# Optimization experiments

Measured on AMD Instinct MI355X. Metric: run time of the kernel, lower is better.

## Reference

```python
import jax, jax.numpy as jnp
import numpy as np


def setup_inputs() -> dict:
    key = jax.random.key(0)
    k1, k2, k3 = jax.random.split(key, 3)
    B, H, W, D, C, F = 2, 96, 128, 64, 32, 32
    images = jax.random.normal(k1, (B, H, W, D, C), dtype=jnp.float32)
    base_plane = jax.random.randint(k2, (B, H, W, 1), 0, 16, dtype=jnp.int32)
    kernel = jax.random.normal(k3, (3, 3, 3, C, F), dtype=jnp.float32) * 0.05
    default_value = jnp.zeros((), dtype=jnp.float32)
    return {"images": images, "base_plane": base_plane,
            "kernel": kernel, "default_value": default_value}


def _sparse_conv3d(images, base_plane, kernel, default_value):
    # images: [B,H,W,D,C] stored depth band per pixel, starting at base_plane
    # base_plane: [B,H,W,1] int, kernel: [KH,KW,KD,C,F]
    B, H, W, D, C = images.shape
    KH, KW, KD, _, F = kernel.shape
    ph, pw, pd = KH // 2, KW // 2, KD // 2
    bp = base_plane[..., 0]  # [B,H,W]

    # pad spatially once; out-of-image neighbors read default_value
    img_pad = jnp.pad(images, ((0, 0), (ph, ph), (pw, pw), (0, 0), (0, 0)))
    bp_pad = jnp.pad(bp, ((0, 0), (ph, ph), (pw, pw)))
    sp_valid_pad = jnp.pad(jnp.ones((H, W), dtype=bool),
                           ((ph, ph), (pw, pw)))

    d_grid = jnp.arange(D)[None, None, None, :]  # [1,1,1,D]
    out = jnp.zeros((B, H, W, D, F), dtype=images.dtype)

    for kh in range(KH):
        for kw in range(KW):
            img_s = img_pad[:, kh:kh + H, kw:kw + W]          # [B,H,W,D,C]
            bp_s = bp_pad[:, kh:kh + H, kw:kw + W]            # [B,H,W]
            sp_valid = sp_valid_pad[kh:kh + H, kw:kw + W]     # [H,W]
            for kd in range(KD):
                # neighbor stored-depth index = (d + bp) + (kd-pd) - bp_neighbor
                idx = d_grid + (bp - bp_s)[:, :, :, None] + (kd - pd)  # [B,H,W,D]
                valid = (idx >= 0) & (idx < D) & sp_valid[None, :, :, None]
                g = jnp.take_along_axis(
                    img_s, jnp.clip(idx, 0, D - 1)[..., None], axis=3)
                val = jnp.where(valid[..., None], g, default_value)
                out = out + jnp.einsum('bhwdc,cf->bhwdf', val,
                                       kernel[kh, kw, kd])
    return out


def reference(images, base_plane, kernel, default_value):
    return _sparse_conv3d(images, base_plane, kernel, default_value)
```

## Files before the change

kernel.cpp:

```cpp
#include <hip/hip_runtime.h>
#include <hip/hip_bf16.h>

#define Bn 2
#define Hn 96
#define Wn 128
#define Dn 64
#define Cn 32
#define Fn 32
#define TH 2
#define TW 8
#define CW (TW + 2)
#define NCOLS (4 * CW)
#define COLSZ (Dn * Cn)

typedef short bf16x8 __attribute__((ext_vector_type(8)));
typedef float f32x4  __attribute__((ext_vector_type(4)));

__device__ __forceinline__ ushort f2bf(float x) {
    __hip_bfloat16 h = __float2bfloat16(x);
    return *reinterpret_cast<ushort*>(&h);
}

__device__ __forceinline__ int swz_off(int r, int slot) {
    return r * 32 + ((slot ^ ((r >> 1) & 3)) << 3);
}

__global__ void prep_kT(const float* __restrict__ kern, ushort* __restrict__ kT) {
    const int e = blockIdx.x * 256 + threadIdx.x;
    if (e >= 30 * Cn * Fn) return;
    const int c  = e & 31;
    const int f  = (e >> 5) & 31;
    const int kk = e >> 10;
    kT[e] = (kk < 27) ? f2bf(kern[kk * (Cn * Fn) + c * Fn + f]) : (ushort)0;
}

__global__ __launch_bounds__(1024, 4) void sconv3d_mfma(
    const float*  __restrict__ img,
    const int*    __restrict__ bp,
    const float*  __restrict__ kern,
    const ushort* __restrict__ kT,
    const float*  __restrict__ dvp,
    float*        __restrict__ out)
{
    __shared__ ushort colS[NCOLS * COLSZ];

    const int blk = blockIdx.x;
    const int wt  = blk % (Wn / TW);
    const int ht  = (blk / (Wn / TW)) % (Hn / TH);
    const int b   = blk / ((Wn / TW) * (Hn / TH));
    const int h0  = ht * TH;
    const int w0  = wt * TW;

    const int tid  = threadIdx.x;
    const int lane = tid & 63;
    const int wave = tid >> 6;
    const int ph   = wave >> 3;
    const int pw   = wave & 7;
    const int h    = h0 + ph;
    const int w    = w0 + pw;

    const int lrow = lane & 15;
    const int lgrp = lane >> 4;

    const float dv  = *dvp;
    const int   bpc = bp[(b * Hn + h) * Wn + w];

    int  sh[9];
    bool tv[9];
#pragma unroll
    for (int kh = 0; kh < 3; ++kh)
#pragma unroll
        for (int kw = 0; kw < 3; ++kw) {
            const int hh = h - 1 + kh;
            const int ww = w - 1 + kw;
            const bool v = (hh >= 0) && (hh < Hn) && (ww >= 0) && (ww < Wn);
            tv[kh * 3 + kw] = v;
            sh[kh * 3 + kw] = v ? (bpc - bp[(b * Hn + hh) * Wn + ww]) : 0;
        }

#pragma unroll
    for (int it = 0; it < 20; ++it) {
        const int e  = it * 1024 + tid;
        const int j  = e >> 9;
        const int sl = e & 511;
        const int hh = h0 - 1 + j / CW;
        const int ww = w0 - 1 + j % CW;
        const bool v = (hh >= 0) && (hh < Hn) && (ww >= 0) && (ww < Wn);
        float4 x = make_float4(0.f, 0.f, 0.f, 0.f);
        if (v) x = *(const float4*)(img +
                     (size_t)((b * Hn + hh) * Wn + ww) * COLSZ + sl * 4);
        ushort4 u;
        u.x = f2bf(x.x); u.y = f2bf(x.y); u.z = f2bf(x.z); u.w = f2bf(x.w);
        *(ushort4*)&colS[j * COLSZ
                         + swz_off(sl >> 3, (sl >> 1) & 3) + (sl & 1) * 4] = u;
    }
    __syncthreads();

    f32x4 acc[4][2];
#pragma unroll
    for (int i = 0; i < 4; ++i)
#pragma unroll
        for (int j = 0; j < 2; ++j) acc[i][j] = (f32x4)0.f;

#pragma unroll
    for (int kh = 0; kh < 3; ++kh) {
#pragma unroll
        for (int kw = 0; kw < 3; ++kw) {
            const int t    = kh * 3 + kw;
            const int s    = sh[t];
            const int kkb  = tv[t] ? t * 3 : 27;
            const ushort* colp = &colS[((ph + kh) * CW + (pw + kw)) * COLSZ];
            bf16x8 bfr[3][2];
#pragma unroll
            for (int kd = 0; kd < 3; ++kd) {
                bfr[kd][0] = *(const bf16x8*)&kT[((kkb + kd) * Fn + lrow)      * Cn + lgrp * 8];
                bfr[kd][1] = *(const bf16x8*)&kT[((kkb + kd) * Fn + lrow + 16) * Cn + lgrp * 8];
            }
            __builtin_amdgcn_s_setprio(1);
#pragma unroll
            for (int kd = 0; kd < 3; ++kd) {
                const int i1 = 16 + lrow + s + kd - 1;
                const int o1 = swz_off(i1, lgrp);
                const bf16x8 a1 = *(const bf16x8*)&colp[o1];
                acc[1][0] = __builtin_amdgcn_mfma_f32_16x16x32_bf16(a1, bfr[kd][0], acc[1][0], 0, 0, 0);
                acc[1][1] = __builtin_amdgcn_mfma_f32_16x16x32_bf16(a1, bfr[kd][1], acc[1][1], 0, 0, 0);
                const bf16x8 a2 = *(const bf16x8*)&colp[o1 + 512];
                acc[2][0] = __builtin_amdgcn_mfma_f32_16x16x32_bf16(a2, bfr[kd][0], acc[2][0], 0, 0, 0);
                acc[2][1] = __builtin_amdgcn_mfma_f32_16x16x32_bf16(a2, bfr[kd][1], acc[2][1], 0, 0, 0);
                {
                    const bool vv = (i1 >= 16);
                    bf16x8 a0 = *(const bf16x8*)&colp[vv ? o1 - 512 : o1];
                    if (!vv) a0 = (bf16x8)0;
                    acc[0][0] = __builtin_amdgcn_mfma_f32_16x16x32_bf16(a0, bfr[kd][0], acc[0][0], 0, 0, 0);
                    acc[0][1] = __builtin_amdgcn_mfma_f32_16x16x32_bf16(a0, bfr[kd][1], acc[0][1], 0, 0, 0);
                }
                {
                    const bool vv = (i1 <= 31);
                    bf16x8 a3 = *(const bf16x8*)&colp[vv ? o1 + 1024 : o1];
                    if (!vv) a3 = (bf16x8)0;
                    acc[3][0] = __builtin_amdgcn_mfma_f32_16x16x32_bf16(a3, bfr[kd][0], acc[3][0], 0, 0, 0);
                    acc[3][1] = __builtin_amdgcn_mfma_f32_16x16x32_bf16(a3, bfr[kd][1], acc[3][1], 0, 0, 0);
                }
            }
            __builtin_amdgcn_s_setprio(0);
        }
    }

    if (dv != 0.0f) {
#pragma unroll
        for (int kh = 0; kh < 3; ++kh)
#pragma unroll
            for (int kw = 0; kw < 3; ++kw) {
                const bool sp = tv[kh * 3 + kw];
                const int  s  = sh[kh * 3 + kw];
                for (int kd = 0; kd < 3; ++kd) {
                    float ks0 = 0.f, ks1 = 0.f;
                    for (int c = 0; c < Cn; ++c) {
                        const float* kp = kern + (size_t)(((kh * 3 + kw) * 3 + kd) * Cn + c) * Fn;
                        ks0 += kp[lrow];
                        ks1 += kp[16 + lrow];
                    }
                    for (int dt = 0; dt < 4; ++dt)
                        for (int j = 0; j < 4; ++j) {
                            const int d   = dt * 16 + lgrp * 4 + j;
                            const int idx = d + s + kd - 1;
                            const bool valid = sp && (idx >= 0) && (idx < Dn);
                            if (!valid) { acc[dt][0][j] += dv * ks0; acc[dt][1][j] += dv * ks1; }
                        }
                }
            }
    }

    const size_t pixbase = ((size_t)(b * Hn + h) * Wn + w) * (Dn * Fn);
#pragma unroll
    for (int dt = 0; dt < 4; ++dt)
#pragma unroll
        for (int ft = 0; ft < 2; ++ft)
#pragma unroll
            for (int j = 0; j < 4; ++j) {
                const int d = dt * 16 + lgrp * 4 + j;
                const int f = ft * 16 + lrow;
                out[pixbase + d * Fn + f] = acc[dt][ft][j];
            }
}

extern "C" void kernel_launch(void* const* d_in, const int* in_sizes, int n_in,
                              void* d_out, int out_size, void* d_ws, size_t ws_size,
                              hipStream_t stream) {
    const float* img  = (const float*)d_in[0];
    const int*   bp   = (const int*)d_in[1];
    const float* kern = (const float*)d_in[2];
    const float* dvp  = (const float*)d_in[3];
    float* out = (float*)d_out;
    ushort* kT = (ushort*)d_ws;

    hipLaunchKernelGGL(prep_kT, dim3(120), dim3(256), 0, stream, kern, kT);

    const int nblk = Bn * (Hn / TH) * (Wn / TW);
    hipLaunchKernelGGL(sconv3d_mfma, dim3(nblk), dim3(1024), 0, stream,
                       img, bp, kern, kT, dvp, out);
}
```

Before: 186.2 us.

## Shrink tile to 1x4 pixels per block with XCD-aware block ordering

Replaces the 2x8-pixel, 1024-thread block with a 1x4-pixel, 256-thread block that stages a 3x6 halo of columns in LDS (18 columns instead of 40). Block IDs are remapped so consecutive blocks spread across the 8 XCDs while neighbouring rows stay on the same XCD for L2 reuse of overlapping halos. The aim is more resident blocks and less LDS per block, traded against higher halo redundancy (4.5 columns loaded per pixel vs 2.5), which adds global and L2 traffic.

```diff
diff --git a/kernel.cpp b/kernel.cpp
--- a/kernel.cpp
+++ b/kernel.cpp
@@ -7,10 +7,9 @@
 #define Dn 64
 #define Cn 32
 #define Fn 32
-#define TH 2
-#define TW 8
-#define CW (TW + 2)
-#define NCOLS (4 * CW)
+#define TWp 4
+#define CWc 6
+#define NC 18
 #define COLSZ (Dn * Cn)
 
 typedef short bf16x8 __attribute__((ext_vector_type(8)));
@@ -34,7 +33,7 @@
     kT[e] = (kk < 27) ? f2bf(kern[kk * (Cn * Fn) + c * Fn + f]) : (ushort)0;
 }
 
-__global__ __launch_bounds__(1024, 4) void sconv3d_mfma(
+__global__ __launch_bounds__(256, 2) void sconv3d_mfma(
     const float*  __restrict__ img,
     const int*    __restrict__ bp,
     const float*  __restrict__ kern,
@@ -42,21 +41,18 @@
     const float*  __restrict__ dvp,
     float*        __restrict__ out)
 {
-    __shared__ ushort colS[NCOLS * COLSZ];
+    __shared__ ushort colS[NC * COLSZ];
 
-    const int blk = blockIdx.x;
-    const int wt  = blk % (Wn / TW);
-    const int ht  = (blk / (Wn / TW)) % (Hn / TH);
-    const int b   = blk / ((Wn / TW) * (Hn / TH));
-    const int h0  = ht * TH;
-    const int w0  = wt * TW;
+    const int sid = (blockIdx.x & 7) * 768 + (blockIdx.x >> 3);
+    const int h   = sid % Hn;
+    const int t2  = sid / Hn;
+    const int wt  = t2 & 31;
+    const int b   = t2 >> 5;
+    const int w0  = wt * TWp;
 
     const int tid  = threadIdx.x;
     const int lane = tid & 63;
-    const int wave = tid >> 6;
-    const int ph   = wave >> 3;
-    const int pw   = wave & 7;
-    const int h    = h0 + ph;
+    const int pw   = tid >> 6;
     const int w    = w0 + pw;
 
     const int lrow = lane & 15;
@@ -79,12 +75,12 @@
         }
 
 #pragma unroll
-    for (int it = 0; it < 20; ++it) {
-        const int e  = it * 1024 + tid;
+    for (int it = 0; it < 36; ++it) {
+        const int e  = it * 256 + tid;
         const int j  = e >> 9;
         const int sl = e & 511;
-        const int hh = h0 - 1 + j / CW;
-        const int ww = w0 - 1 + j % CW;
+        const int hh = h - 1 + j / CWc;
+        const int ww = w0 - 1 + j % CWc;
         const bool v = (hh >= 0) && (hh < Hn) && (ww >= 0) && (ww < Wn);
         float4 x = make_float4(0.f, 0.f, 0.f, 0.f);
         if (v) x = *(const float4*)(img +
@@ -109,7 +105,7 @@
             const int t    = kh * 3 + kw;
             const int s    = sh[t];
             const int kkb  = tv[t] ? t * 3 : 27;
-            const ushort* colp = &colS[((ph + kh) * CW + (pw + kw)) * COLSZ];
+            const ushort* colp = &colS[(kh * CWc + (pw + kw)) * COLSZ];
             bf16x8 bfr[3][2];
 #pragma unroll
             for (int kd = 0; kd < 3; ++kd) {
@@ -196,7 +192,7 @@
 
     hipLaunchKernelGGL(prep_kT, dim3(120), dim3(256), 0, stream, kern, kT);
 
-    const int nblk = Bn * (Hn / TH) * (Wn / TW);
-    hipLaunchKernelGGL(sconv3d_mfma, dim3(nblk), dim3(1024), 0, stream,
+    const int nblk = Bn * Hn * (Wn / TWp);
+    hipLaunchKernelGGL(sconv3d_mfma, dim3(nblk), dim3(256), 0, stream,
                        img, bp, kern, kT, dvp, out);
 }
```

Result: slower. 263.2 us (+41.3%).

## Remap blocks per XCD, simplify halo load addressing, use packed bf16 convert

Applied to the files above, without the earlier changes.

Changes the block-index decode so consecutive blocks dispatched to the same XCD cover neighbouring width tiles, improving L2 reuse of the overlapping halo columns. Rewrites the halo staging loop with precomputed base pointers and per-iteration compile-time offsets, removing per-element div/mod and bounds math. Replaces four scalar float-to-bf16 conversions with two packed v_cvt_pk_bf16_f32 instructions. Relies on the grid being a multiple of 8 and on the XCD round-robin dispatch assumption.

```diff
diff --git a/kernel.cpp b/kernel.cpp
--- a/kernel.cpp
+++ b/kernel.cpp
@@ -21,6 +21,13 @@
     return *reinterpret_cast<ushort*>(&h);
 }
 
+__device__ __forceinline__ uint2 f4bf(float4 v) {
+    uint2 r;
+    asm("v_cvt_pk_bf16_f32 %0, %1, %2" : "=v"(r.x) : "v"(v.x), "v"(v.y));
+    asm("v_cvt_pk_bf16_f32 %0, %1, %2" : "=v"(r.y) : "v"(v.z), "v"(v.w));
+    return r;
+}
+
 __device__ __forceinline__ int swz_off(int r, int slot) {
     return r * 32 + ((slot ^ ((r >> 1) & 3)) << 3);
 }
@@ -44,10 +51,13 @@
 {
     __shared__ ushort colS[NCOLS * COLSZ];
 
-    const int blk = blockIdx.x;
-    const int wt  = blk % (Wn / TW);
-    const int ht  = (blk / (Wn / TW)) % (Hn / TH);
-    const int b   = blk / ((Wn / TW) * (Hn / TH));
+    const int xcd = blockIdx.x & 7;
+    const int i   = blockIdx.x >> 3;
+    const int ht  = i % (Hn / TH);
+    const int q   = i / (Hn / TH);
+    const int cI  = xcd * 4 + q;
+    const int wt  = cI & 15;
+    const int b   = cI >> 4;
     const int h0  = ht * TH;
     const int w0  = wt * TW;
 
@@ -78,29 +88,34 @@
             sh[kh * 3 + kw] = v ? (bpc - bp[(b * Hn + hh) * Wn + ww]) : 0;
         }
 
-#pragma unroll
-    for (int it = 0; it < 20; ++it) {
-        const int e  = it * 1024 + tid;
-        const int j  = e >> 9;
-        const int sl = e & 511;
-        const int hh = h0 - 1 + j / CW;
-        const int ww = w0 - 1 + j % CW;
-        const bool v = (hh >= 0) && (hh < Hn) && (ww >= 0) && (ww < Wn);
-        float4 x = make_float4(0.f, 0.f, 0.f, 0.f);
-        if (v) x = *(const float4*)(img +
-                     (size_t)((b * Hn + hh) * Wn + ww) * COLSZ + sl * 4);
-        ushort4 u;
-        u.x = f2bf(x.x); u.y = f2bf(x.y); u.z = f2bf(x.z); u.w = f2bf(x.w);
-        *(ushort4*)&colS[j * COLSZ
-                         + swz_off(sl >> 3, (sl >> 1) & 3) + (sl & 1) * 4] = u;
+    {
+        const int jbase = tid >> 9;
+        const int sl    = tid & 511;
+        const int swzT  = swz_off(sl >> 3, (sl >> 1) & 3) + (sl & 1) * 4;
+        const bool wl_ok = !((w0 == 0) && (jbase == 0));
+        const bool wr_ok = !((w0 == Wn - TW) && (jbase == 1));
+        const float*  gbase = img + (size_t)((b * Hn + (h0 - 1)) * Wn + (w0 - 1) + jbase) * COLSZ + sl * 4;
+        ushort*       lbase = colS + jbase * COLSZ + swzT;
+#pragma unroll
+        for (int it = 0; it < 20; ++it) {
+            const int r  = (2 * it) / 10;
+            const int cc = (2 * it) % 10;
+            const int hh = h0 - 1 + r;
+            const bool v = (hh >= 0) && (hh < Hn) &&
+                           (cc == 0 ? wl_ok : (cc == 8 ? wr_ok : true));
+            float4 x = make_float4(0.f, 0.f, 0.f, 0.f);
+            if (v) x = *(const float4*)(gbase + (size_t)(r * Wn + cc) * COLSZ);
+            const uint2 u = f4bf(x);
+            *(uint2*)(lbase + 2 * it * COLSZ) = u;
+        }
     }
     __syncthreads();
 
     f32x4 acc[4][2];
 #pragma unroll
-    for (int i = 0; i < 4; ++i)
-#pragma unroll
-        for (int j = 0; j < 2; ++j) acc[i][j] = (f32x4)0.f;
+    for (int i2 = 0; i2 < 4; ++i2)
+#pragma unroll
+        for (int j2 = 0; j2 < 2; ++j2) acc[i2][j2] = (f32x4)0.f;
 
 #pragma unroll
     for (int kh = 0; kh < 3; ++kh) {
```

Result: faster. 176.0 us, median of 2 (-5.5%).
